# Kernel tuning notes

Hardware: AMD Instinct MI355X
Metric: run time of the kernel (lower is better)

Reference implementation:

```python
import jax, jax.numpy as jnp
import numpy as np

B, Q, C_IN, C_OUT, S, NH = 4, 4096, 256, 256, 8, 8
H_FEAT, W_FEAT = 128, 128


def grid_sample_bilinear(img, grid):
    """torch.nn.functional.grid_sample, mode='bilinear', padding_mode='zeros', align_corners=False.
    img: [B, C, H, W]; grid: [B, Hg, Wg, 2] with (x, y) in [-1, 1]. Returns [B, C, Hg, Wg]."""
    b, c, h, w = img.shape
    gx = (grid[..., 0] + 1.0) * (w * 0.5) - 0.5
    gy = (grid[..., 1] + 1.0) * (h * 0.5) - 0.5
    x0f = jnp.floor(gx)
    y0f = jnp.floor(gy)
    x0 = x0f.astype(jnp.int32)
    y0 = y0f.astype(jnp.int32)
    wx1 = (gx - x0f)[:, None]  # [B,1,Hg,Wg]
    wy1 = (gy - y0f)[:, None]
    img_flat = img.reshape(b, c, h * w)

    def corner(xi, yi):
        inb = ((xi >= 0) & (xi < w) & (yi >= 0) & (yi < h)).astype(img.dtype)
        idx = jnp.clip(yi, 0, h - 1) * w + jnp.clip(xi, 0, w - 1)
        v = jax.vmap(lambda im, ix: im[:, ix.reshape(-1)])(img_flat, idx)  # [B,C,Hg*Wg]
        return v.reshape(b, c, *xi.shape[1:]) * inb[:, None]

    v00 = corner(x0, y0)
    v01 = corner(x0 + 1, y0)
    v10 = corner(x0, y0 + 1)
    v11 = corner(x0 + 1, y0 + 1)
    return (v00 * (1 - wx1) * (1 - wy1) + v01 * wx1 * (1 - wy1)
            + v10 * (1 - wx1) * wy1 + v11 * wx1 * wy1)


def setup_inputs() -> dict:
    key = jax.random.key(0)
    ks = jax.random.split(key, 16)
    sc = 0.02
    return {
        "queries": jax.random.normal(ks[0], (B, Q, C_IN), jnp.float32),
        "keys": jax.random.normal(ks[1], (B, C_IN, H_FEAT, W_FEAT), jnp.float32),
        "values": jax.random.normal(ks[2], (B, C_IN, H_FEAT, W_FEAT), jnp.float32),
        "W_loc": jax.random.normal(ks[3], (C_IN, S * 2), jnp.float32) * sc,
        "b_loc": jnp.zeros((S * 2,), jnp.float32),
        "W_q": jax.random.normal(ks[4], (C_IN, C_OUT), jnp.float32) * sc,
        "b_q": jnp.zeros((C_OUT,), jnp.float32),
        "W_k": jax.random.normal(ks[5], (C_OUT, C_IN), jnp.float32) * sc,
        "b_k": jnp.zeros((C_OUT,), jnp.float32),
        "W_v": jax.random.normal(ks[6], (C_OUT, C_IN), jnp.float32) * sc,
        "b_v": jnp.zeros((C_OUT,), jnp.float32),
        "W_o": jax.random.normal(ks[7], (C_OUT, C_OUT), jnp.float32) * sc,
        "b_o": jnp.zeros((C_OUT,), jnp.float32),
    }


def reference(queries, keys, values, W_loc, b_loc, W_q, b_q, W_k, b_k, W_v, b_v, W_o, b_o):
    b, q, _ = queries.shape
    d = C_OUT // NH
    # predicted sampling locations in [-1, 1]: [B, Q, S, 2]
    loc = jnp.tanh(queries @ W_loc + b_loc).reshape(b, q, S, 2)
    # query projection -> [B, Q, NH, d]
    qh = (queries @ W_q + b_q).reshape(b, q, NH, d)
    # 1x1 conv projections of feature maps
    k_proj = jnp.einsum('oc,bchw->bohw', W_k, keys) + b_k[None, :, None, None]
    v_proj = jnp.einsum('oc,bchw->bohw', W_v, values) + b_v[None, :, None, None]
    # deformable sampling: [B, C_OUT, Q, S] -> [B, Q, NH, d, S]
    ks_ = grid_sample_bilinear(k_proj, loc).transpose(0, 2, 1, 3).reshape(b, q, NH, d, S)
    vs_ = grid_sample_bilinear(v_proj, loc).transpose(0, 2, 1, 3).reshape(b, q, NH, d, S)
    # per-query attention over S sampled points (note: scale uses full out_channels)
    attn = jnp.einsum('bqhd,bqhds->bqhs', qh, ks_) / np.sqrt(C_OUT).astype(np.float32)
    attn = jax.nn.softmax(attn, axis=-1)
    out = jnp.einsum('bqhds,bqhs->bqhd', vs_, attn).reshape(b, q, C_OUT)
    return out @ W_o + b_o
```

## Files before the change

### kernel.cpp

```cpp
#include <hip/hip_runtime.h>
#include <hip/hip_bf16.h>

#define NB 4
#define NQ 4096
#define CI 256
#define CO 256
#define NS 8
#define HFEAT 128
#define WFEAT 128
#define NPIX (HFEAT * WFEAT)

typedef short bf16x8 __attribute__((ext_vector_type(8)));
typedef float f32x4 __attribute__((ext_vector_type(4)));

__device__ __forceinline__ unsigned short f2b(float x) {
    union { float f; unsigned u; } v; v.f = x;
    unsigned r = v.u + 0x7fff + ((v.u >> 16) & 1);
    return (unsigned short)(r >> 16);
}
__device__ __forceinline__ float b2f(unsigned short x) {
    union { unsigned u; float f; } v; v.u = ((unsigned)x) << 16;
    return v.f;
}
__device__ __forceinline__ void b2f2(unsigned u, float& a, float& b) {
    union { unsigned x; float f; } va, vb;
    va.x = u << 16;
    vb.x = u & 0xffff0000u;
    a = va.f; b = vb.f;
}
__device__ __forceinline__ void gload16(const void* g, void* l) {
    __builtin_amdgcn_global_load_lds((const __attribute__((address_space(1))) void*)g,
                                     (__attribute__((address_space(3))) void*)l, 16, 0, 0);
}

__global__ __launch_bounds__(256) void k_prep_w(const float* __restrict__ Wk,
                                                const float* __restrict__ Wv,
                                                const float* __restrict__ Wq,
                                                const float* __restrict__ Wo,
                                                unsigned short* __restrict__ out) {
    int mat = blockIdx.y;
    int base = blockIdx.x * 1024 + threadIdx.x * 4;
    const float* src = (mat == 0) ? Wk : (mat == 1) ? Wv : (mat == 2) ? Wq : Wo;
    unsigned short* dst = out + (size_t)mat * 65536;
    if (mat < 2) {
#pragma unroll
        for (int i = 0; i < 4; ++i) dst[base + i] = f2b(src[base + i]);
    } else {
#pragma unroll
        for (int i = 0; i < 4; ++i) {
            int oi = base + i;
            int o = oi >> 8, c = oi & 255;
            dst[oi] = f2b(src[c * 256 + o]);
        }
    }
}

__global__ __launch_bounds__(256) void k_cvt(const float* __restrict__ in,
                                             unsigned short* __restrict__ out) {
    size_t i = ((size_t)blockIdx.x * 256 + threadIdx.x) * 8;
    float4 a = *reinterpret_cast<const float4*>(in + i);
    float4 b = *reinterpret_cast<const float4*>(in + i + 4);
    union { uint2 u2[2]; unsigned short h[8]; } pk;
    pk.h[0] = f2b(a.x); pk.h[1] = f2b(a.y); pk.h[2] = f2b(a.z); pk.h[3] = f2b(a.w);
    pk.h[4] = f2b(b.x); pk.h[5] = f2b(b.y); pk.h[6] = f2b(b.z); pk.h[7] = f2b(b.w);
    *reinterpret_cast<uint4*>(out + i) = *reinterpret_cast<uint4*>(&pk);
}

__global__ __launch_bounds__(256) void k_loc(const float* __restrict__ q,
                                             const float* __restrict__ Wl,
                                             const float* __restrict__ bl,
                                             float* __restrict__ loc) {
    __shared__ float qs[32][260];
    __shared__ float wlt[16][260];
    int t = threadIdx.x;
    int row0 = blockIdx.x * 32;
    {
        int rr = t >> 6;
        int c4 = (t & 63) * 4;
#pragma unroll
        for (int i = 0; i < 8; ++i) {
            int r = i * 4 + rr;
            *reinterpret_cast<float4*>(&qs[r][c4]) =
                *reinterpret_cast<const float4*>(q + (size_t)(row0 + r) * CI + c4);
        }
    }
    {
        int c = t;
#pragma unroll
        for (int col = 0; col < 16; ++col) wlt[col][c] = Wl[c * 16 + col];
    }
    __syncthreads();
    int r = t & 31;
    int cg = t >> 5;
    float a0 = bl[cg], a1 = bl[cg + 8];
    for (int c4 = 0; c4 < 256; c4 += 4) {
        float4 qv = *reinterpret_cast<const float4*>(&qs[r][c4]);
        float4 w0 = *reinterpret_cast<const float4*>(&wlt[cg][c4]);
        float4 w1 = *reinterpret_cast<const float4*>(&wlt[cg + 8][c4]);
        a0 = fmaf(qv.x, w0.x, a0); a0 = fmaf(qv.y, w0.y, a0);
        a0 = fmaf(qv.z, w0.z, a0); a0 = fmaf(qv.w, w0.w, a0);
        a1 = fmaf(qv.x, w1.x, a1); a1 = fmaf(qv.y, w1.y, a1);
        a1 = fmaf(qv.z, w1.z, a1); a1 = fmaf(qv.w, w1.w, a1);
    }
    loc[(size_t)(row0 + r) * 16 + cg] = tanhf(a0);
    loc[(size_t)(row0 + r) * 16 + cg + 8] = tanhf(a1);
}

template <int OUT_BF16>
__global__ __launch_bounds__(256) void k_gemm(const unsigned short* __restrict__ A,
                                              const unsigned short* __restrict__ Bt,
                                              const float* __restrict__ bias,
                                              void* __restrict__ outp) {
    __shared__ unsigned short As[128][32];
    __shared__ unsigned short Bs[128][32];
    int t = threadIdx.x;
    int w = t >> 6, l = t & 63;
    int bm = blockIdx.x >> 1, bc = blockIdx.x & 1;
    int m0 = bm * 128, n0 = bc * 128;
    int wr = w >> 1, wc = w & 1;

    f32x4 acc[4][4];
#pragma unroll
    for (int n = 0; n < 4; ++n) {
        float bv = bias[n0 + wc * 64 + n * 16 + (l & 15)];
#pragma unroll
        for (int m = 0; m < 4; ++m) acc[m][n] = f32x4{bv, bv, bv, bv};
    }

    int ar = wr * 64 + (l & 15);
    int br = wc * 64 + (l & 15);
    int kq = (l >> 4) * 8;
    int srow = (l >> 2);
    int scol = (l & 3) * 8;

    for (int kk = 0; kk < 8; ++kk) {
        int k0 = kk * 32;
#pragma unroll
        for (int j = 0; j < 2; ++j) {
            int row = w * 32 + j * 16 + srow;
            gload16(A + (size_t)(m0 + row) * CI + k0 + scol, &As[w * 32 + j * 16][0]);
            gload16(Bt + (size_t)(n0 + row) * CI + k0 + scol, &Bs[w * 32 + j * 16][0]);
        }
        __syncthreads();
        bf16x8 af[4], bfr[4];
#pragma unroll
        for (int m = 0; m < 4; ++m) af[m] = *reinterpret_cast<const bf16x8*>(&As[ar + m * 16][kq]);
#pragma unroll
        for (int n = 0; n < 4; ++n) bfr[n] = *reinterpret_cast<const bf16x8*>(&Bs[br + n * 16][kq]);
#pragma unroll
        for (int m = 0; m < 4; ++m)
#pragma unroll
            for (int n = 0; n < 4; ++n)
                acc[m][n] = __builtin_amdgcn_mfma_f32_16x16x32_bf16(af[m], bfr[n], acc[m][n], 0, 0, 0);
        __syncthreads();
    }

    int rbase = m0 + wr * 64 + (l >> 4) * 4;
    int cbase = n0 + wc * 64 + (l & 15);
#pragma unroll
    for (int m = 0; m < 4; ++m)
#pragma unroll
        for (int n = 0; n < 4; ++n)
#pragma unroll
            for (int r = 0; r < 4; ++r) {
                size_t row = rbase + m * 16 + r;
                size_t col = cbase + n * 16;
                if (OUT_BF16)
                    ((unsigned short*)outp)[row * CO + col] = f2b(acc[m][n][r]);
                else
                    ((float*)outp)[row * CO + col] = acc[m][n][r];
            }
}

__global__ __launch_bounds__(256) void k_proj(const float* __restrict__ keys,
                                              const float* __restrict__ values,
                                              const unsigned short* __restrict__ wbuf,
                                              const float* __restrict__ bK,
                                              const float* __restrict__ bV,
                                              unsigned short* __restrict__ kp,
                                              unsigned short* __restrict__ vp) {
    __shared__ unsigned short As[128][40];
    __shared__ unsigned short Bs[2][128][32];
    int blk = ((blockIdx.x & 7) << 8) | (blockIdx.x >> 3);
    int map = blk >> 10;
    int rem = blk & 1023;
    int b = rem >> 8;
    int rem2 = rem & 255;
    int pix0 = (rem2 >> 1) * 128;
    int o0 = (rem2 & 1) * 128;
    const float* X = (map ? values : keys) + (size_t)b * (CI * NPIX);
    const unsigned short* W = wbuf + (size_t)map * 65536;
    const float* bias = map ? bV : bK;
    unsigned short* outp = (map ? vp : kp) + (size_t)b * (NPIX * CO);

    int t = threadIdx.x;
    int w = t >> 6, l = t & 63;
    int wr = w >> 1, wc = w & 1;

    f32x4 acc[4][4];
#pragma unroll
    for (int n = 0; n < 4; ++n) {
        float bv = bias[o0 + wc * 64 + n * 16 + (l & 15)];
#pragma unroll
        for (int m = 0; m < 4; ++m) acc[m][n] = f32x4{bv, bv, bv, bv};
    }

    int cp0 = t >> 5;
    int pxl = 4 * (t & 31);
    int fx = ((t & 31) ^ ((t & 31) >> 2)) & 3;
    int colA = cp0 ^ (fx << 2);
    int colB = (cp0 + 8) ^ (fx << 2);
    const float* Xp = X + pix0 + pxl;

    int srow = l >> 2, scol = (l & 3) * 8;

    int ar = wr * 64 + (l & 15);
    int br = wc * 64 + (l & 15);
    int g = l >> 4;
    int kq = g * 8;

    float4 fa0, fa1, fa2, fa3;

#define LOADA(kk)                                                         \
    {                                                                     \
        const float* p_ = Xp + (size_t)((kk) * 32 + 2 * cp0) * NPIX;      \
        fa0 = *(const float4*)(p_);                                       \
        fa1 = *(const float4*)(p_ + NPIX);                                \
        fa2 = *(const float4*)(p_ + 16 * NPIX);                           \
        fa3 = *(const float4*)(p_ + 17 * NPIX);                           \
    }
#define WRITEA()                                                          \
    {                                                                     \
        const float* q0_ = (const float*)&fa0;                            \
        const float* q1_ = (const float*)&fa1;                            \
        const float* q2_ = (const float*)&fa2;                            \
        const float* q3_ = (const float*)&fa3;                            \
        _Pragma("unroll")                                                 \
        for (int j = 0; j < 4; ++j) {                                     \
            unsigned d0_ = (unsigned)f2b(q0_[j]) | ((unsigned)f2b(q1_[j]) << 16); \
            unsigned d1_ = (unsigned)f2b(q2_[j]) | ((unsigned)f2b(q3_[j]) << 16); \
            unsigned* rp_ = (unsigned*)&As[pxl + j][0];                   \
            rp_[colA] = d0_;                                              \
            rp_[colB] = d1_;                                              \
        }                                                                 \
    }
#define LOADB(kk, buf)                                                    \
    {                                                                     \
        int k0_ = (kk) * 32;                                              \
        _Pragma("unroll")                                                 \
        for (int j = 0; j < 2; ++j) {                                     \
            int row_ = w * 32 + j * 16;                                   \
            gload16(W + (size_t)(o0 + row_ + srow) * CI + k0_ + scol,     \
                    &Bs[buf][row_][0]);                                   \
        }                                                                 \
    }

    LOADA(0);
    LOADB(0, 0);
    WRITEA();
    __syncthreads();

    for (int kk = 0; kk < 8; ++kk) {
        if (kk < 7) {
            LOADA(kk + 1);
            LOADB(kk + 1, (kk + 1) & 1);
        }
        bf16x8 af[4], bfr[4];
#pragma unroll
        for (int m = 0; m < 4; ++m) {
            int p = ar + m * 16;
            int gm = (g ^ (((p >> 2) ^ (p >> 4)) & 3)) * 8;
            af[m] = *reinterpret_cast<const bf16x8*>(&As[p][gm]);
        }
#pragma unroll
        for (int n = 0; n < 4; ++n)
            bfr[n] = *reinterpret_cast<const bf16x8*>(&Bs[kk & 1][br + n * 16][kq]);
#pragma unroll
        for (int m = 0; m < 4; ++m)
#pragma unroll
            for (int n = 0; n < 4; ++n)
                acc[m][n] = __builtin_amdgcn_mfma_f32_16x16x32_bf16(af[m], bfr[n], acc[m][n], 0, 0, 0);
        __syncthreads();
        if (kk < 7) {
            WRITEA();
            __syncthreads();
        }
    }

    int rbase = wr * 64 + (l >> 4) * 4;
    int cbase = o0 + wc * 64 + (l & 15);
#pragma unroll
    for (int m = 0; m < 4; ++m)
#pragma unroll
        for (int n = 0; n < 4; ++n)
#pragma unroll
            for (int r = 0; r < 4; ++r) {
                size_t row = (size_t)pix0 + rbase + m * 16 + r;
                size_t col = cbase + n * 16;
                outp[row * CO + col] = f2b(acc[m][n][r]);
            }
#undef LOADA
#undef WRITEA
#undef LOADB
}

__global__ __launch_bounds__(256) void k_attn(const unsigned short* __restrict__ kp,
                                              const unsigned short* __restrict__ vp,
                                              const unsigned short* __restrict__ qh,
                                              const float* __restrict__ loc,
                                              unsigned short* __restrict__ aout) {
    int t = threadIdx.x;
    int wv = t >> 6, l = t & 63;
    int blk = blockIdx.x;
    int xcd = blk & 7;
    int b = xcd >> 1;
    int idx = ((blk >> 3) << 1) | (xcd & 1);
    int bq = (b << 12) | (idx << 2) | wv;

    float qv[4];
    {
        uint2 qr = *reinterpret_cast<const uint2*>(qh + (size_t)bq * CO + l * 4);
        b2f2(qr.x, qv[0], qv[1]);
        b2f2(qr.y, qv[2], qv[3]);
    }
    const unsigned short* kb = kp + (size_t)b * NPIX * CO;
    const unsigned short* vb = vp + (size_t)b * NPIX * CO;
    const float* lq = loc + (size_t)bq * (NS * 2);
    int choff = l * 4;

    float m = -3.0e38f, lsum = 0.f;
    float o0 = 0.f, o1 = 0.f, o2 = 0.f, o3 = 0.f;

#pragma unroll
    for (int s = 0; s < NS; ++s) {
        float x = lq[2 * s];
        float y = lq[2 * s + 1];
        float gx = (x + 1.f) * (WFEAT * 0.5f) - 0.5f;
        float gy = (y + 1.f) * (HFEAT * 0.5f) - 0.5f;
        float x0f = floorf(gx), y0f = floorf(gy);
        int x0 = (int)x0f, y0 = (int)y0f;
        float wx1 = gx - x0f, wy1 = gy - y0f;
        float wx0 = 1.f - wx1, wy0 = 1.f - wy1;
        bool xa = (x0 >= 0) && (x0 < WFEAT);
        bool xb = (x0 + 1 >= 0) && (x0 + 1 < WFEAT);
        bool ya = (y0 >= 0) && (y0 < HFEAT);
        bool yb = (y0 + 1 >= 0) && (y0 + 1 < HFEAT);
        size_t i00 = (size_t)(y0 * WFEAT + x0) * CO + choff;

        uint2 z = make_uint2(0u, 0u);
        uint2 k00 = z, k01 = z, k10 = z, k11 = z;
        uint2 v00 = z, v01 = z, v10 = z, v11 = z;
        if (xa && ya) { k00 = *(const uint2*)(kb + i00);                 v00 = *(const uint2*)(vb + i00); }
        if (xb && ya) { k01 = *(const uint2*)(kb + i00 + CO);            v01 = *(const uint2*)(vb + i00 + CO); }
        if (xa && yb) { k10 = *(const uint2*)(kb + i00 + WFEAT * CO);    v10 = *(const uint2*)(vb + i00 + WFEAT * CO); }
        if (xb && yb) { k11 = *(const uint2*)(kb + i00 + (WFEAT+1)*CO);  v11 = *(const uint2*)(vb + i00 + (WFEAT+1)*CO); }

        float a0, a1, b0, b1, c0, c1, d0, d1;
        float ks[4], vs[4];
        b2f2(k00.x, a0, a1); b2f2(k01.x, b0, b1); b2f2(k10.x, c0, c1); b2f2(k11.x, d0, d1);
        ks[0] = fmaf(fmaf(b0, wx1, a0 * wx0), wy0, fmaf(d0, wx1, c0 * wx0) * wy1);
        ks[1] = fmaf(fmaf(b1, wx1, a1 * wx0), wy0, fmaf(d1, wx1, c1 * wx0) * wy1);
        b2f2(k00.y, a0, a1); b2f2(k01.y, b0, b1); b2f2(k10.y, c0, c1); b2f2(k11.y, d0, d1);
        ks[2] = fmaf(fmaf(b0, wx1, a0 * wx0), wy0, fmaf(d0, wx1, c0 * wx0) * wy1);
        ks[3] = fmaf(fmaf(b1, wx1, a1 * wx0), wy0, fmaf(d1, wx1, c1 * wx0) * wy1);
        b2f2(v00.x, a0, a1); b2f2(v01.x, b0, b1); b2f2(v10.x, c0, c1); b2f2(v11.x, d0, d1);
        vs[0] = fmaf(fmaf(b0, wx1, a0 * wx0), wy0, fmaf(d0, wx1, c0 * wx0) * wy1);
        vs[1] = fmaf(fmaf(b1, wx1, a1 * wx0), wy0, fmaf(d1, wx1, c1 * wx0) * wy1);
        b2f2(v00.y, a0, a1); b2f2(v01.y, b0, b1); b2f2(v10.y, c0, c1); b2f2(v11.y, d0, d1);
        vs[2] = fmaf(fmaf(b0, wx1, a0 * wx0), wy0, fmaf(d0, wx1, c0 * wx0) * wy1);
        vs[3] = fmaf(fmaf(b1, wx1, a1 * wx0), wy0, fmaf(d1, wx1, c1 * wx0) * wy1);

        float p = fmaf(qv[0], ks[0], fmaf(qv[1], ks[1], fmaf(qv[2], ks[2], qv[3] * ks[3])));
        p += __shfl_xor(p, 1);
        p += __shfl_xor(p, 2);
        p += __shfl_xor(p, 4);
        float lg = p * 0.0625f;

        float nm = fmaxf(m, lg);
        float sc = __expf(m - nm);
        float wgt = __expf(lg - nm);
        lsum = fmaf(lsum, sc, wgt);
        o0 = fmaf(o0, sc, wgt * vs[0]);
        o1 = fmaf(o1, sc, wgt * vs[1]);
        o2 = fmaf(o2, sc, wgt * vs[2]);
        o3 = fmaf(o3, sc, wgt * vs[3]);
        m = nm;
    }

    float inv = 1.f / lsum;
    uint2 pk;
    pk.x = ((unsigned)f2b(o0 * inv)) | (((unsigned)f2b(o1 * inv)) << 16);
    pk.y = ((unsigned)f2b(o2 * inv)) | (((unsigned)f2b(o3 * inv)) << 16);
    *reinterpret_cast<uint2*>(aout + (size_t)bq * CO + choff) = pk;
}

extern "C" void kernel_launch(void* const* d_in, const int* in_sizes, int n_in,
                              void* d_out, int out_size, void* d_ws, size_t ws_size,
                              hipStream_t stream) {
    (void)in_sizes; (void)n_in; (void)out_size; (void)ws_size;
    const float* queries = (const float*)d_in[0];
    const float* keys    = (const float*)d_in[1];
    const float* values  = (const float*)d_in[2];
    const float* W_loc   = (const float*)d_in[3];
    const float* b_loc   = (const float*)d_in[4];
    const float* W_q     = (const float*)d_in[5];
    const float* b_q     = (const float*)d_in[6];
    const float* W_k     = (const float*)d_in[7];
    const float* b_k     = (const float*)d_in[8];
    const float* W_v     = (const float*)d_in[9];
    const float* b_v     = (const float*)d_in[10];
    const float* W_o     = (const float*)d_in[11];
    const float* b_o     = (const float*)d_in[12];
    float* out = (float*)d_out;

    char* ws = (char*)d_ws;
    unsigned short* kp   = (unsigned short*)(ws);
    unsigned short* vp   = (unsigned short*)(ws + 33554432);
    unsigned short* qbf  = (unsigned short*)(ws + 67108864);
    unsigned short* aout = (unsigned short*)(ws + 67108864);
    unsigned short* qh   = (unsigned short*)(ws + 75497472);
    float* locb          = (float*)(ws + 83886080);
    unsigned short* wbuf = (unsigned short*)(ws + 84934656);

    k_prep_w<<<dim3(64, 4), 256, 0, stream>>>(W_k, W_v, W_q, W_o, wbuf);
    k_cvt<<<dim3(2048), 256, 0, stream>>>(queries, qbf);
    k_loc<<<dim3(512), 256, 0, stream>>>(queries, W_loc, b_loc, locb);
    k_gemm<1><<<dim3(256), 256, 0, stream>>>(qbf, wbuf + 131072, b_q, qh);
    k_proj<<<dim3(2048), 256, 0, stream>>>(keys, values, wbuf, b_k, b_v, kp, vp);
    k_attn<<<dim3(NB * NQ / 4), 256, 0, stream>>>(kp, vp, qh, locb, aout);
    k_gemm<0><<<dim3(256), 256, 0, stream>>>(aout, wbuf + 196608, b_o, out);
}
```

Baseline: 124.2 us.

## Fuse query bf16 conversion into loc kernel and batch attention gathers

The standalone query conversion kernel is folded into the location-prediction kernel, which already stages the queries in shared memory, saving a launch and one re-read of the queries. The attention kernel is restructured to compute all sampling coordinates first and then issue all key gathers together, followed by a plain (non-online) softmax and then all value gathers. Bilinear weights are applied to per-corner dot products rather than interpolating keys first. This exposes more memory-level parallelism per thread at the cost of higher register pressure, and it also uses the hardware packed bf16 convert instruction.

```diff
diff --git a/kernel.cpp b/kernel.cpp
--- a/kernel.cpp
+++ b/kernel.cpp
@@ -27,6 +27,11 @@
     va.x = u << 16;
     vb.x = u & 0xffff0000u;
     a = va.f; b = vb.f;
+}
+__device__ __forceinline__ unsigned cvtpk(float a, float b) {
+    unsigned r;
+    asm("v_cvt_pk_bf16_f32 %0, %1, %2" : "=v"(r) : "v"(a), "v"(b));
+    return r;
 }
 __device__ __forceinline__ void gload16(const void* g, void* l) {
     __builtin_amdgcn_global_load_lds((const __attribute__((address_space(1))) void*)g,
@@ -55,21 +60,11 @@
     }
 }
 
-__global__ __launch_bounds__(256) void k_cvt(const float* __restrict__ in,
-                                             unsigned short* __restrict__ out) {
-    size_t i = ((size_t)blockIdx.x * 256 + threadIdx.x) * 8;
-    float4 a = *reinterpret_cast<const float4*>(in + i);
-    float4 b = *reinterpret_cast<const float4*>(in + i + 4);
-    union { uint2 u2[2]; unsigned short h[8]; } pk;
-    pk.h[0] = f2b(a.x); pk.h[1] = f2b(a.y); pk.h[2] = f2b(a.z); pk.h[3] = f2b(a.w);
-    pk.h[4] = f2b(b.x); pk.h[5] = f2b(b.y); pk.h[6] = f2b(b.z); pk.h[7] = f2b(b.w);
-    *reinterpret_cast<uint4*>(out + i) = *reinterpret_cast<uint4*>(&pk);
-}
-
-__global__ __launch_bounds__(256) void k_loc(const float* __restrict__ q,
-                                             const float* __restrict__ Wl,
-                                             const float* __restrict__ bl,
-                                             float* __restrict__ loc) {
+__global__ __launch_bounds__(256) void k_qprep(const float* __restrict__ q,
+                                               const float* __restrict__ Wl,
+                                               const float* __restrict__ bl,
+                                               float* __restrict__ loc,
+                                               unsigned short* __restrict__ qbf) {
     __shared__ float qs[32][260];
     __shared__ float wlt[16][260];
     int t = threadIdx.x;
@@ -90,6 +85,19 @@
         for (int col = 0; col < 16; ++col) wlt[col][c] = Wl[c * 16 + col];
     }
     __syncthreads();
+    {
+        int rr = t >> 3, cc = (t & 7) * 32;
+        unsigned short* dst = qbf + (size_t)(row0 + rr) * CI + cc;
+#pragma unroll
+        for (int i = 0; i < 4; ++i) {
+            uint4 pk4;
+            pk4.x = cvtpk(qs[rr][cc + i * 8 + 0], qs[rr][cc + i * 8 + 1]);
+            pk4.y = cvtpk(qs[rr][cc + i * 8 + 2], qs[rr][cc + i * 8 + 3]);
+            pk4.z = cvtpk(qs[rr][cc + i * 8 + 4], qs[rr][cc + i * 8 + 5]);
+            pk4.w = cvtpk(qs[rr][cc + i * 8 + 6], qs[rr][cc + i * 8 + 7]);
+            *reinterpret_cast<uint4*>(dst + i * 8) = pk4;
+        }
+    }
     int r = t & 31;
     int cg = t >> 5;
     float a0 = bl[cg], a1 = bl[cg + 8];
@@ -323,75 +331,101 @@
         b2f2(qr.x, qv[0], qv[1]);
         b2f2(qr.y, qv[2], qv[3]);
     }
-    const unsigned short* kb = kp + (size_t)b * NPIX * CO;
-    const unsigned short* vb = vp + (size_t)b * NPIX * CO;
+    const unsigned short* kb = kp + (size_t)b * NPIX * CO + l * 4;
+    const unsigned short* vb = vp + (size_t)b * NPIX * CO + l * 4;
     const float* lq = loc + (size_t)bq * (NS * 2);
-    int choff = l * 4;
-
-    float m = -3.0e38f, lsum = 0.f;
-    float o0 = 0.f, o1 = 0.f, o2 = 0.f, o3 = 0.f;
-
+
+    int i00[NS];
+    float w00[NS], w01[NS], w10[NS], w11[NS];
+    unsigned msks = 0;
 #pragma unroll
     for (int s = 0; s < NS; ++s) {
-        float x = lq[2 * s];
-        float y = lq[2 * s + 1];
-        float gx = (x + 1.f) * (WFEAT * 0.5f) - 0.5f;
-        float gy = (y + 1.f) * (HFEAT * 0.5f) - 0.5f;
+        float gx = (lq[2 * s] + 1.f) * (WFEAT * 0.5f) - 0.5f;
+        float gy = (lq[2 * s + 1] + 1.f) * (HFEAT * 0.5f) - 0.5f;
         float x0f = floorf(gx), y0f = floorf(gy);
         int x0 = (int)x0f, y0 = (int)y0f;
         float wx1 = gx - x0f, wy1 = gy - y0f;
         float wx0 = 1.f - wx1, wy0 = 1.f - wy1;
-        bool xa = (x0 >= 0) && (x0 < WFEAT);
-        bool xb = (x0 + 1 >= 0) && (x0 + 1 < WFEAT);
-        bool ya = (y0 >= 0) && (y0 < HFEAT);
-        bool yb = (y0 + 1 >= 0) && (y0 + 1 < HFEAT);
-        size_t i00 = (size_t)(y0 * WFEAT + x0) * CO + choff;
-
+        w00[s] = wx0 * wy0; w01[s] = wx1 * wy0;
+        w10[s] = wx0 * wy1; w11[s] = wx1 * wy1;
+        unsigned xa = (unsigned)x0 < WFEAT, xb = (unsigned)(x0 + 1) < WFEAT;
+        unsigned ya = (unsigned)y0 < HFEAT, yb = (unsigned)(y0 + 1) < HFEAT;
+        msks |= ((xa & ya) | ((xb & ya) << 1) | ((xa & yb) << 2) | ((xb & yb) << 3)) << (4 * s);
+        i00[s] = (y0 * WFEAT + x0) * CO;
+    }
+
+    uint2 cr[NS][4];
+#pragma unroll
+    for (int s = 0; s < NS; ++s) {
         uint2 z = make_uint2(0u, 0u);
-        uint2 k00 = z, k01 = z, k10 = z, k11 = z;
-        uint2 v00 = z, v01 = z, v10 = z, v11 = z;
-        if (xa && ya) { k00 = *(const uint2*)(kb + i00);                 v00 = *(const uint2*)(vb + i00); }
-        if (xb && ya) { k01 = *(const uint2*)(kb + i00 + CO);            v01 = *(const uint2*)(vb + i00 + CO); }
-        if (xa && yb) { k10 = *(const uint2*)(kb + i00 + WFEAT * CO);    v10 = *(const uint2*)(vb + i00 + WFEAT * CO); }
-        if (xb && yb) { k11 = *(const uint2*)(kb + i00 + (WFEAT+1)*CO);  v11 = *(const uint2*)(vb + i00 + (WFEAT+1)*CO); }
-
-        float a0, a1, b0, b1, c0, c1, d0, d1;
-        float ks[4], vs[4];
-        b2f2(k00.x, a0, a1); b2f2(k01.x, b0, b1); b2f2(k10.x, c0, c1); b2f2(k11.x, d0, d1);
-        ks[0] = fmaf(fmaf(b0, wx1, a0 * wx0), wy0, fmaf(d0, wx1, c0 * wx0) * wy1);
-        ks[1] = fmaf(fmaf(b1, wx1, a1 * wx0), wy0, fmaf(d1, wx1, c1 * wx0) * wy1);
-        b2f2(k00.y, a0, a1); b2f2(k01.y, b0, b1); b2f2(k10.y, c0, c1); b2f2(k11.y, d0, d1);
-        ks[2] = fmaf(fmaf(b0, wx1, a0 * wx0), wy0, fmaf(d0, wx1, c0 * wx0) * wy1);
-        ks[3] = fmaf(fmaf(b1, wx1, a1 * wx0), wy0, fmaf(d1, wx1, c1 * wx0) * wy1);
-        b2f2(v00.x, a0, a1); b2f2(v01.x, b0, b1); b2f2(v10.x, c0, c1); b2f2(v11.x, d0, d1);
-        vs[0] = fmaf(fmaf(b0, wx1, a0 * wx0), wy0, fmaf(d0, wx1, c0 * wx0) * wy1);
-        vs[1] = fmaf(fmaf(b1, wx1, a1 * wx0), wy0, fmaf(d1, wx1, c1 * wx0) * wy1);
-        b2f2(v00.y, a0, a1); b2f2(v01.y, b0, b1); b2f2(v10.y, c0, c1); b2f2(v11.y, d0, d1);
-        vs[2] = fmaf(fmaf(b0, wx1, a0 * wx0), wy0, fmaf(d0, wx1, c0 * wx0) * wy1);
-        vs[3] = fmaf(fmaf(b1, wx1, a1 * wx0), wy0, fmaf(d1, wx1, c1 * wx0) * wy1);
-
-        float p = fmaf(qv[0], ks[0], fmaf(qv[1], ks[1], fmaf(qv[2], ks[2], qv[3] * ks[3])));
+        cr[s][0] = z; cr[s][1] = z; cr[s][2] = z; cr[s][3] = z;
+        unsigned m4 = msks >> (4 * s);
+        if (m4 & 1) cr[s][0] = *(const uint2*)(kb + i00[s]);
+        if (m4 & 2) cr[s][1] = *(const uint2*)(kb + i00[s] + CO);
+        if (m4 & 4) cr[s][2] = *(const uint2*)(kb + i00[s] + WFEAT * CO);
+        if (m4 & 8) cr[s][3] = *(const uint2*)(kb + i00[s] + (WFEAT + 1) * CO);
+    }
+    float lg[NS];
+#pragma unroll
+    for (int s = 0; s < NS; ++s) {
+        float d[4];
+#pragma unroll
+        for (int c = 0; c < 4; ++c) {
+            float a0, a1, a2, a3;
+            b2f2(cr[s][c].x, a0, a1);
+            b2f2(cr[s][c].y, a2, a3);
+            d[c] = fmaf(qv[0], a0, fmaf(qv[1], a1, fmaf(qv[2], a2, qv[3] * a3)));
+        }
+        float p = fmaf(d[0], w00[s], fmaf(d[1], w01[s], fmaf(d[2], w10[s], d[3] * w11[s])));
         p += __shfl_xor(p, 1);
         p += __shfl_xor(p, 2);
         p += __shfl_xor(p, 4);
-        float lg = p * 0.0625f;
-
-        float nm = fmaxf(m, lg);
-        float sc = __expf(m - nm);
-        float wgt = __expf(lg - nm);
-        lsum = fmaf(lsum, sc, wgt);
-        o0 = fmaf(o0, sc, wgt * vs[0]);
-        o1 = fmaf(o1, sc, wgt * vs[1]);
-        o2 = fmaf(o2, sc, wgt * vs[2]);
-        o3 = fmaf(o3, sc, wgt * vs[3]);
-        m = nm;
-    }
-
-    float inv = 1.f / lsum;
+        lg[s] = p * 0.0625f;
+    }
+    float mx = fmaxf(fmaxf(fmaxf(lg[0], lg[1]), fmaxf(lg[2], lg[3])),
+                     fmaxf(fmaxf(lg[4], lg[5]), fmaxf(lg[6], lg[7])));
+    float ws[NS];
+    float sum = 0.f;
+#pragma unroll
+    for (int s = 0; s < NS; ++s) { ws[s] = __expf(lg[s] - mx); sum += ws[s]; }
+    float inv = 1.f / sum;
+#pragma unroll
+    for (int s = 0; s < NS; ++s) ws[s] *= inv;
+
+#pragma unroll
+    for (int s = 0; s < NS; ++s) {
+        uint2 z = make_uint2(0u, 0u);
+        cr[s][0] = z; cr[s][1] = z; cr[s][2] = z; cr[s][3] = z;
+        unsigned m4 = msks >> (4 * s);
+        if (m4 & 1) cr[s][0] = *(const uint2*)(vb + i00[s]);
+        if (m4 & 2) cr[s][1] = *(const uint2*)(vb + i00[s] + CO);
+        if (m4 & 4) cr[s][2] = *(const uint2*)(vb + i00[s] + WFEAT * CO);
+        if (m4 & 8) cr[s][3] = *(const uint2*)(vb + i00[s] + (WFEAT + 1) * CO);
+    }
+    float o0 = 0.f, o1 = 0.f, o2 = 0.f, o3 = 0.f;
+#pragma unroll
+    for (int s = 0; s < NS; ++s) {
+        float f0 = ws[s] * w00[s], f1 = ws[s] * w01[s];
+        float f2 = ws[s] * w10[s], f3 = ws[s] * w11[s];
+        float a0, a1, a2, a3;
+        b2f2(cr[s][0].x, a0, a1); b2f2(cr[s][0].y, a2, a3);
+        o0 = fmaf(f0, a0, o0); o1 = fmaf(f0, a1, o1);
+        o2 = fmaf(f0, a2, o2); o3 = fmaf(f0, a3, o3);
+        b2f2(cr[s][1].x, a0, a1); b2f2(cr[s][1].y, a2, a3);
+        o0 = fmaf(f1, a0, o0); o1 = fmaf(f1, a1, o1);
+        o2 = fmaf(f1, a2, o2); o3 = fmaf(f1, a3, o3);
+        b2f2(cr[s][2].x, a0, a1); b2f2(cr[s][2].y, a2, a3);
+        o0 = fmaf(f2, a0, o0); o1 = fmaf(f2, a1, o1);
+        o2 = fmaf(f2, a2, o2); o3 = fmaf(f2, a3, o3);
+        b2f2(cr[s][3].x, a0, a1); b2f2(cr[s][3].y, a2, a3);
+        o0 = fmaf(f3, a0, o0); o1 = fmaf(f3, a1, o1);
+        o2 = fmaf(f3, a2, o2); o3 = fmaf(f3, a3, o3);
+    }
+
     uint2 pk;
-    pk.x = ((unsigned)f2b(o0 * inv)) | (((unsigned)f2b(o1 * inv)) << 16);
-    pk.y = ((unsigned)f2b(o2 * inv)) | (((unsigned)f2b(o3 * inv)) << 16);
-    *reinterpret_cast<uint2*>(aout + (size_t)bq * CO + choff) = pk;
+    pk.x = cvtpk(o0, o1);
+    pk.y = cvtpk(o2, o3);
+    *reinterpret_cast<uint2*>(aout + (size_t)bq * CO + l * 4) = pk;
 }
 
 extern "C" void kernel_launch(void* const* d_in, const int* in_sizes, int n_in,
@@ -423,8 +457,7 @@
     unsigned short* wbuf = (unsigned short*)(ws + 84934656);
 
     k_prep_w<<<dim3(64, 4), 256, 0, stream>>>(W_k, W_v, W_q, W_o, wbuf);
-    k_cvt<<<dim3(2048), 256, 0, stream>>>(queries, qbf);
-    k_loc<<<dim3(512), 256, 0, stream>>>(queries, W_loc, b_loc, locb);
+    k_qprep<<<dim3(512), 256, 0, stream>>>(queries, W_loc, b_loc, locb, qbf);
     k_gemm<1><<<dim3(256), 256, 0, stream>>>(qbf, wbuf + 131072, b_q, qh);
     k_proj<<<dim3(2048), 256, 0, stream>>>(keys, values, wbuf, b_k, b_v, kp, vp);
     k_attn<<<dim3(NB * NQ / 4), 256, 0, stream>>>(kp, vp, qh, locb, aout);
```

After: 118.2 us, median of 2. 1.05x faster.
